# Optimization experiments

Measured on AMD Instinct MI355X. Metric: run time of the kernel, lower is better.

The kernel has to match this reference:

```python
import jax, jax.numpy as jnp
import numpy as np

SCALE_FACTOR = 8.0  # sqrt(head_dim=64)

def setup_inputs() -> dict:
    key = jax.random.key(0)
    kq, kk, kv = jax.random.split(key, 3)
    BH, S, D = 64, 2048, 64  # batch*heads, seq_len, head_dim
    q = jax.random.normal(kq, (BH, S, D), dtype=jnp.float32)
    k = jax.random.normal(kk, (BH, S, D), dtype=jnp.float32)
    v = jax.random.normal(kv, (BH, S, D), dtype=jnp.float32)
    return {"q": q, "k": k, "v": v}

def reference(q, k, v):
    # qk = q @ k^T, scaled, softmax over keys, (dropout p=0 == identity), @ v
    scores = jnp.einsum("bqd,bkd->bqk", q, k) / SCALE_FACTOR  # [BH, S, S]
    attn = jax.nn.softmax(scores, axis=-1)
    out = jnp.einsum("bqk,bkd->bqd", attn, v)  # [BH, S, D]
    return out
```

## Files before the change

### kernel.cpp

```cpp
#include <hip/hip_runtime.h>
#include <hip/hip_bf16.h>


typedef __attribute__((ext_vector_type(8))) short short8;
typedef __attribute__((ext_vector_type(4))) short short4v;
typedef __attribute__((ext_vector_type(4))) float float4v;

#define S_LEN 2048
#define D_DIM 64
#define BH_N  64
#define LOG2E 1.4426950408889634f
#define CLF   (0.125f * LOG2E)

__device__ __forceinline__ unsigned int fpack2_fast(float a, float b) {
    unsigned int ua = __builtin_bit_cast(unsigned int, a) + 0x8000u;
    unsigned int ub = __builtin_bit_cast(unsigned int, b) + 0x8000u;
    return __builtin_amdgcn_perm(ub, ua, 0x07060302);
}
__device__ __forceinline__ unsigned int fpack2_trunc(float a, float b) {
    return __builtin_amdgcn_perm(__builtin_bit_cast(unsigned int, b),
                                 __builtin_bit_cast(unsigned int, a),
                                 0x07060302);
}
__device__ __forceinline__ void load16_lds(const unsigned short* g, unsigned short* l) {
    __builtin_amdgcn_global_load_lds(
        (const __attribute__((address_space(1))) unsigned int*)g,
        (__attribute__((address_space(3))) unsigned int*)l,
        16, 0, 0);
}

__global__ void __launch_bounds__(256) prep(const float* __restrict__ k,
                                            const float* __restrict__ v,
                                            unsigned short* __restrict__ kbf,
                                            unsigned short* __restrict__ vt) {
    __shared__ unsigned short T[64 * 66];
    const int b = blockIdx.x;
    const int t = threadIdx.x;
    if (b & 1) {
        const int kb = b >> 1;
        const size_t i = ((size_t)kb * 256 + t) * 16;
        #pragma unroll
        for (int j = 0; j < 2; ++j) {
            const float4 a0 = *(const float4*)(k + i + j * 8);
            const float4 a1 = *(const float4*)(k + i + j * 8 + 4);
            uint4 o;
            o.x = fpack2_fast(a0.x, a0.y); o.y = fpack2_fast(a0.z, a0.w);
            o.z = fpack2_fast(a1.x, a1.y); o.w = fpack2_fast(a1.z, a1.w);
            *(uint4*)(kbf + i + j * 8) = o;
        }
        return;
    }
    const int idx = b >> 1;
    const int kt = idx & 31, bh = idx >> 5;
    const float* Vg = v + ((size_t)bh * S_LEN + kt * 64) * D_DIM;
    #pragma unroll
    for (int it = 0; it < 4; ++it) {
        const int row = it * 16 + (t >> 4);
        const int col = (t & 15) * 4;
        const float4 f = *(const float4*)(Vg + row * 64 + col);
        unsigned int* p = (unsigned int*)&T[row * 66 + col];
        p[0] = fpack2_fast(f.x, f.y);
        p[1] = fpack2_fast(f.z, f.w);
    }
    __syncthreads();
    const int d  = t >> 2;
    const int kg = t & 3;
    unsigned int w[8];
    #pragma unroll
    for (int j = 0; j < 8; ++j) {
        const unsigned int lo = T[(kg * 16 + 2 * j)     * 66 + d];
        const unsigned int hi = T[(kg * 16 + 2 * j + 1) * 66 + d];
        w[j] = __builtin_amdgcn_perm(hi, lo, 0x05040100);
    }
    unsigned short* out = vt + ((size_t)bh * 64 + d) * S_LEN + kt * 64 + kg * 16;
    uint4 o0; o0.x = w[0]; o0.y = w[1]; o0.z = w[2]; o0.w = w[3];
    uint4 o1; o1.x = w[4]; o1.y = w[5]; o1.z = w[6]; o1.w = w[7];
    *(uint4*)(out)     = o0;
    *(uint4*)(out + 8) = o1;
}

__global__ void __launch_bounds__(256, 4) attn_fwd5(
        const float* __restrict__ q, const unsigned short* __restrict__ kbf,
        const unsigned short* __restrict__ vt, float* __restrict__ out) {
    __shared__ __align__(16) unsigned short Klds[2][64 * 64];
    __shared__ __align__(16) unsigned short Vlds[2][64 * 64];

    const int tid  = threadIdx.x;
    const int lane = tid & 63;
    const int wave = tid >> 6;
    const int l16  = lane & 15;
    const int quad = lane >> 4;
    const int rsw  = l16 & 7;

    const int bh    = blockIdx.y;
    const int qbase = blockIdx.x * 128;

    const unsigned short* Kb = kbf + (size_t)bh * S_LEN * D_DIM;
    const unsigned short* Vb = vt  + (size_t)bh * D_DIM * S_LEN;

    short8 qf[2][2];
    #pragma unroll
    for (int s = 0; s < 2; ++s) {
        const int qg = qbase + s * 64 + wave * 16 + l16;
        const float* Qr = q + ((size_t)bh * S_LEN + qg) * D_DIM;
        #pragma unroll
        for (int h = 0; h < 2; ++h) {
            const float4 a = *(const float4*)(Qr + h * 32 + quad * 8);
            const float4 b = *(const float4*)(Qr + h * 32 + quad * 8 + 4);
            uint4 w;
            w.x = fpack2_fast(a.x * CLF, a.y * CLF);
            w.y = fpack2_fast(a.z * CLF, a.w * CLF);
            w.z = fpack2_fast(b.x * CLF, b.y * CLF);
            w.w = fpack2_fast(b.z * CLF, b.w * CLF);
            qf[s][h] = __builtin_bit_cast(short8, w);
        }
    }

    const int srow0  = wave * 16 + (lane >> 3);
    const int schunk = (lane & 7) ^ (lane >> 3);
    const int dsoff  = wave * 1024 + lane * 8;

    float4v acc[2][4];
    #pragma unroll
    for (int s = 0; s < 2; ++s)
        #pragma unroll
        for (int dt = 0; dt < 4; ++dt) acc[s][dt] = (float4v){0.f, 0.f, 0.f, 0.f};
    float l_acc[2] = {0.f, 0.f};

    auto stage = [&](int kt, int buf) {
        #pragma unroll
        for (int ss = 0; ss < 2; ++ss) {
            const int row = srow0 + ss * 8;
            load16_lds(Kb + ((size_t)(kt * 64 + row)) * 64 + schunk * 8,
                       &Klds[buf][dsoff + ss * 512]);
            load16_lds(Vb + (size_t)row * S_LEN + kt * 64 + schunk * 8,
                       &Vlds[buf][dsoff + ss * 512]);
        }
    };

    auto tile = [&](int buf) {
        float4v st[2][4];
        #pragma unroll
        for (int ks = 0; ks < 4; ++ks) {
            const unsigned short* kr = &Klds[buf][(ks * 16 + l16) * 64];
            const int p0 = ((quad ^ rsw) * 8);
            const short8 kf0 = *(const short8*)(kr + p0);
            const short8 kf1 = *(const short8*)(kr + (p0 ^ 32));
            #pragma unroll
            for (int s = 0; s < 2; ++s) {
                float4v z = (float4v){0.f, 0.f, 0.f, 0.f};
                z = __builtin_amdgcn_mfma_f32_16x16x32_bf16(kf0, qf[s][0], z, 0, 0, 0);
                z = __builtin_amdgcn_mfma_f32_16x16x32_bf16(kf1, qf[s][1], z, 0, 0, 0);
                st[s][ks] = z;
            }
        }
        short4v pf[2][4];
        #pragma unroll
        for (int s = 0; s < 2; ++s) {
            #pragma unroll
            for (int ks = 0; ks < 4; ++ks) {
                const float p0 = __builtin_amdgcn_exp2f(st[s][ks][0]);
                const float p1 = __builtin_amdgcn_exp2f(st[s][ks][1]);
                const float p2 = __builtin_amdgcn_exp2f(st[s][ks][2]);
                const float p3 = __builtin_amdgcn_exp2f(st[s][ks][3]);
                l_acc[s] += (p0 + p1) + (p2 + p3);
                uint2 u; u.x = fpack2_trunc(p0, p1); u.y = fpack2_trunc(p2, p3);
                pf[s][ks] = __builtin_bit_cast(short4v, u);
            }
        }
        #pragma unroll
        for (int dt = 0; dt < 4; ++dt) {
            const unsigned short* vrow = &Vlds[buf][(dt * 16 + l16) * 64 + (quad & 1) * 4];
            #pragma unroll
            for (int ks = 0; ks < 4; ++ks) {
                const int pos16 = (ks * 2 + (quad >> 1)) ^ rsw;
                const short4v vf = *(const short4v*)(vrow + pos16 * 8);
                #pragma unroll
                for (int s = 0; s < 2; ++s)
                    acc[s][dt] = __builtin_amdgcn_mfma_f32_16x16x16bf16_1k(vf, pf[s][ks], acc[s][dt], 0, 0, 0);
            }
        }
    };

    stage(0, 0);
    #pragma unroll 1
    for (int kt = 0; kt < S_LEN / 64; kt += 2) {
        __syncthreads();
        stage(kt + 1, 1);
        tile(0);
        __syncthreads();
        if (kt + 2 < S_LEN / 64) stage(kt + 2, 0);
        tile(1);
    }

    #pragma unroll
    for (int s = 0; s < 2; ++s) {
        float l = l_acc[s];
        l += __shfl_xor(l, 16, 64);
        l += __shfl_xor(l, 32, 64);
        const float inv = 1.0f / l;
        const int qg = qbase + s * 64 + wave * 16 + l16;
        float* Or = out + ((size_t)bh * S_LEN + qg) * D_DIM;
        #pragma unroll
        for (int dt = 0; dt < 4; ++dt) {
            float4 o;
            o.x = acc[s][dt][0] * inv; o.y = acc[s][dt][1] * inv;
            o.z = acc[s][dt][2] * inv; o.w = acc[s][dt][3] * inv;
            *(float4*)(Or + dt * 16 + quad * 4) = o;
        }
    }
}

#define KSTRIDE 72
__global__ void __launch_bounds__(256) attn_fwd(
        const float* __restrict__ q, const float* __restrict__ k,
        const float* __restrict__ v, float* __restrict__ out) {
    __shared__ __align__(16) unsigned short Klds[64 * KSTRIDE];
    __shared__ __align__(16) unsigned short Vlds[64 * KSTRIDE];
    const int tid  = threadIdx.x;
    const int lane = tid & 63;
    const int wave = tid >> 6;
    const int l16  = lane & 15;
    const int quad = lane >> 4;
    const int bh    = blockIdx.y;
    const int qg    = blockIdx.x * 64 + wave * 16 + l16;
    const float* Qr = q + ((size_t)bh * S_LEN + qg) * D_DIM;
    const float* Kb = k + (size_t)bh * S_LEN * D_DIM;
    const float* Vb = v + (size_t)bh * S_LEN * D_DIM;
    short8 qf[2];
    #pragma unroll
    for (int h = 0; h < 2; ++h) {
        const float4 a = *(const float4*)(Qr + h * 32 + quad * 8);
        const float4 b = *(const float4*)(Qr + h * 32 + quad * 8 + 4);
        uint4 w;
        w.x = fpack2_fast(a.x * CLF, a.y * CLF);
        w.y = fpack2_fast(a.z * CLF, a.w * CLF);
        w.z = fpack2_fast(b.x * CLF, b.y * CLF);
        w.w = fpack2_fast(b.z * CLF, b.w * CLF);
        qf[h] = __builtin_bit_cast(short8, w);
    }
    float4v acc[4];
    #pragma unroll
    for (int dt = 0; dt < 4; ++dt) acc[dt] = (float4v){0.f, 0.f, 0.f, 0.f};
    float l_acc = 0.f;
    for (int kt = 0; kt < S_LEN / 64; ++kt) {
        __syncthreads();
        {
            const float* Kg = Kb + (size_t)kt * 64 * D_DIM;
            #pragma unroll
            for (int i = 0; i < 4; ++i) {
                const int idx = tid + i * 256;
                const int row = idx >> 4;
                const int col = (idx & 15) << 2;
                const float4 f = *(const float4*)(Kg + row * 64 + col);
                uint2 w; w.x = fpack2_fast(f.x, f.y); w.y = fpack2_fast(f.z, f.w);
                *(uint2*)(&Klds[row * KSTRIDE + col]) = w;
            }
        }
        {
            const float* Vg = Vb + (size_t)kt * 64 * D_DIM;
            #pragma unroll
            for (int it = 0; it < 2; ++it) {
                const int rp   = (tid & 15) + (it << 4);
                const int cg   = tid >> 4;
                const int row0 = rp * 2;
                const int col  = cg * 4;
                const float4 a = *(const float4*)(Vg + row0 * 64 + col);
                const float4 b = *(const float4*)(Vg + (row0 + 1) * 64 + col);
                *(unsigned int*)(&Vlds[(col + 0) * KSTRIDE + row0]) = fpack2_fast(a.x, b.x);
                *(unsigned int*)(&Vlds[(col + 1) * KSTRIDE + row0]) = fpack2_fast(a.y, b.y);
                *(unsigned int*)(&Vlds[(col + 2) * KSTRIDE + row0]) = fpack2_fast(a.z, b.z);
                *(unsigned int*)(&Vlds[(col + 3) * KSTRIDE + row0]) = fpack2_fast(a.w, b.w);
            }
        }
        __syncthreads();
        float4v st[4];
        #pragma unroll
        for (int ks = 0; ks < 4; ++ks) {
            const unsigned short* kr = &Klds[(ks * 16 + l16) * KSTRIDE + quad * 8];
            const short8 kf0 = *(const short8*)(kr);
            const short8 kf1 = *(const short8*)(kr + 32);
            float4v z = (float4v){0.f, 0.f, 0.f, 0.f};
            z = __builtin_amdgcn_mfma_f32_16x16x32_bf16(kf0, qf[0], z, 0, 0, 0);
            z = __builtin_amdgcn_mfma_f32_16x16x32_bf16(kf1, qf[1], z, 0, 0, 0);
            st[ks] = z;
        }
        short4v pf[4];
        #pragma unroll
        for (int ks = 0; ks < 4; ++ks) {
            const float p0 = __builtin_amdgcn_exp2f(st[ks][0]);
            const float p1 = __builtin_amdgcn_exp2f(st[ks][1]);
            const float p2 = __builtin_amdgcn_exp2f(st[ks][2]);
            const float p3 = __builtin_amdgcn_exp2f(st[ks][3]);
            l_acc += (p0 + p1) + (p2 + p3);
            uint2 u; u.x = fpack2_trunc(p0, p1); u.y = fpack2_trunc(p2, p3);
            pf[ks] = __builtin_bit_cast(short4v, u);
        }
        #pragma unroll
        for (int dt = 0; dt < 4; ++dt) {
            const unsigned short* vr = &Vlds[(dt * 16 + l16) * KSTRIDE + quad * 4];
            #pragma unroll
            for (int ks = 0; ks < 4; ++ks) {
                const short4v vf = *(const short4v*)(vr + ks * 16);
                acc[dt] = __builtin_amdgcn_mfma_f32_16x16x16bf16_1k(vf, pf[ks], acc[dt], 0, 0, 0);
            }
        }
    }
    float l = l_acc;
    l += __shfl_xor(l, 16, 64);
    l += __shfl_xor(l, 32, 64);
    const float inv = 1.0f / l;
    float* Or = out + ((size_t)bh * S_LEN + qg) * D_DIM;
    #pragma unroll
    for (int dt = 0; dt < 4; ++dt) {
        float4 o;
        o.x = acc[dt][0] * inv; o.y = acc[dt][1] * inv;
        o.z = acc[dt][2] * inv; o.w = acc[dt][3] * inv;
        *(float4*)(Or + dt * 16 + quad * 4) = o;
    }
}

extern "C" void kernel_launch(void* const* d_in, const int* in_sizes, int n_in,
                              void* d_out, int out_size, void* d_ws, size_t ws_size,
                              hipStream_t stream) {
    const float* q = (const float*)d_in[0];
    const float* k = (const float*)d_in[1];
    const float* v = (const float*)d_in[2];
    float* out = (float*)d_out;
    const size_t need = (size_t)2 * BH_N * S_LEN * D_DIM * sizeof(unsigned short);
    if (ws_size >= need) {
        unsigned short* kbf = (unsigned short*)d_ws;
        unsigned short* vtp = kbf + (size_t)BH_N * S_LEN * D_DIM;
        prep<<<dim3(4096), 256, 0, stream>>>(k, v, kbf, vtp);
        attn_fwd5<<<dim3(S_LEN / 128, BH_N), 256, 0, stream>>>(q, kbf, vtp, out);
    } else {
        attn_fwd<<<dim3(S_LEN / 64, BH_N), 256, 0, stream>>>(q, k, v, out);
    }
}
```

Before: 217.6 us.

## Drop LDS staging; load K and permuted V fragments directly from global into registers

The attention kernel no longer stages K and V tiles through double-buffered shared memory with barriers. Each wave now loads its own MFMA fragments straight from global memory. The prep kernel writes V-transpose with its keys permuted so that the PV product can use the wider 16x16x32 bf16 MFMA with 8-element fragments in place of 16x16x16. This removes LDS traffic and __syncthreads, but every wave now re-reads K and V from global memory or L2 with no cross-wave sharing and only compiler-driven prefetch.

Result: slower. 447.1 us (+105.5%).

```diff
diff --git a/kernel.cpp b/kernel.cpp
--- a/kernel.cpp
+++ b/kernel.cpp
@@ -21,12 +21,6 @@
     return __builtin_amdgcn_perm(__builtin_bit_cast(unsigned int, b),
                                  __builtin_bit_cast(unsigned int, a),
                                  0x07060302);
-}
-__device__ __forceinline__ void load16_lds(const unsigned short* g, unsigned short* l) {
-    __builtin_amdgcn_global_load_lds(
-        (const __attribute__((address_space(1))) unsigned int*)g,
-        (__attribute__((address_space(3))) unsigned int*)l,
-        16, 0, 0);
 }
 
 __global__ void __launch_bounds__(256) prep(const float* __restrict__ k,
@@ -64,33 +58,32 @@
     }
     __syncthreads();
     const int d  = t >> 2;
-    const int kg = t & 3;
-    unsigned int w[8];
-    #pragma unroll
-    for (int j = 0; j < 8; ++j) {
-        const unsigned int lo = T[(kg * 16 + 2 * j)     * 66 + d];
-        const unsigned int hi = T[(kg * 16 + 2 * j + 1) * 66 + d];
-        w[j] = __builtin_amdgcn_perm(hi, lo, 0x05040100);
-    }
-    unsigned short* out = vt + ((size_t)bh * 64 + d) * S_LEN + kt * 64 + kg * 16;
-    uint4 o0; o0.x = w[0]; o0.y = w[1]; o0.z = w[2]; o0.w = w[3];
-    uint4 o1; o1.x = w[4]; o1.y = w[5]; o1.z = w[6]; o1.w = w[7];
-    *(uint4*)(out)     = o0;
-    *(uint4*)(out + 8) = o1;
-}
-
-__global__ void __launch_bounds__(256, 4) attn_fwd5(
+    const int cg = t & 3;
+    unsigned int w8[8];
+    #pragma unroll
+    for (int cc = 0; cc < 2; ++cc) {
+        const int c   = cg * 2 + cc;
+        const int kb0 = (c >> 2) * 32 + (c & 3) * 4;
+        w8[cc*4+0] = __builtin_amdgcn_perm(T[(kb0+ 1)*66+d], T[(kb0+ 0)*66+d], 0x05040100);
+        w8[cc*4+1] = __builtin_amdgcn_perm(T[(kb0+ 3)*66+d], T[(kb0+ 2)*66+d], 0x05040100);
+        w8[cc*4+2] = __builtin_amdgcn_perm(T[(kb0+17)*66+d], T[(kb0+16)*66+d], 0x05040100);
+        w8[cc*4+3] = __builtin_amdgcn_perm(T[(kb0+19)*66+d], T[(kb0+18)*66+d], 0x05040100);
+    }
+    unsigned short* outp = vt + ((size_t)bh * 64 + d) * S_LEN + kt * 64 + cg * 16;
+    uint4 o0; o0.x = w8[0]; o0.y = w8[1]; o0.z = w8[2]; o0.w = w8[3];
+    uint4 o1; o1.x = w8[4]; o1.y = w8[5]; o1.z = w8[6]; o1.w = w8[7];
+    *(uint4*)(outp)     = o0;
+    *(uint4*)(outp + 8) = o1;
+}
+
+__global__ void __launch_bounds__(256, 4) attn_fwd6(
         const float* __restrict__ q, const unsigned short* __restrict__ kbf,
         const unsigned short* __restrict__ vt, float* __restrict__ out) {
-    __shared__ __align__(16) unsigned short Klds[2][64 * 64];
-    __shared__ __align__(16) unsigned short Vlds[2][64 * 64];
-
     const int tid  = threadIdx.x;
     const int lane = tid & 63;
     const int wave = tid >> 6;
     const int l16  = lane & 15;
     const int quad = lane >> 4;
-    const int rsw  = l16 & 7;
 
     const int bh    = blockIdx.y;
     const int qbase = blockIdx.x * 128;
@@ -116,9 +109,8 @@
         }
     }
 
-    const int srow0  = wave * 16 + (lane >> 3);
-    const int schunk = (lane & 7) ^ (lane >> 3);
-    const int dsoff  = wave * 1024 + lane * 8;
+    const unsigned short* Krow = Kb + (size_t)l16 * 64 + quad * 8;
+    const unsigned short* Vrow = Vb + (size_t)l16 * S_LEN + quad * 8;
 
     float4v acc[2][4];
     #pragma unroll
@@ -127,70 +119,63 @@
         for (int dt = 0; dt < 4; ++dt) acc[s][dt] = (float4v){0.f, 0.f, 0.f, 0.f};
     float l_acc[2] = {0.f, 0.f};
 
-    auto stage = [&](int kt, int buf) {
-        #pragma unroll
-        for (int ss = 0; ss < 2; ++ss) {
-            const int row = srow0 + ss * 8;
-            load16_lds(Kb + ((size_t)(kt * 64 + row)) * 64 + schunk * 8,
-                       &Klds[buf][dsoff + ss * 512]);
-            load16_lds(Vb + (size_t)row * S_LEN + kt * 64 + schunk * 8,
-                       &Vlds[buf][dsoff + ss * 512]);
-        }
-    };
-
-    auto tile = [&](int buf) {
+    #pragma unroll 2
+    for (int kt = 0; kt < S_LEN / 64; ++kt) {
+        const unsigned short* kp = Krow + (size_t)(kt * 64) * 64;
+        short8 kf[4][2];
+        #pragma unroll
+        for (int ks = 0; ks < 4; ++ks) {
+            kf[ks][0] = *(const short8*)(kp + ks * 16 * 64);
+            kf[ks][1] = *(const short8*)(kp + ks * 16 * 64 + 32);
+        }
         float4v st[2][4];
         #pragma unroll
         for (int ks = 0; ks < 4; ++ks) {
-            const unsigned short* kr = &Klds[buf][(ks * 16 + l16) * 64];
-            const int p0 = ((quad ^ rsw) * 8);
-            const short8 kf0 = *(const short8*)(kr + p0);
-            const short8 kf1 = *(const short8*)(kr + (p0 ^ 32));
             #pragma unroll
             for (int s = 0; s < 2; ++s) {
                 float4v z = (float4v){0.f, 0.f, 0.f, 0.f};
-                z = __builtin_amdgcn_mfma_f32_16x16x32_bf16(kf0, qf[s][0], z, 0, 0, 0);
-                z = __builtin_amdgcn_mfma_f32_16x16x32_bf16(kf1, qf[s][1], z, 0, 0, 0);
+                z = __builtin_amdgcn_mfma_f32_16x16x32_bf16(kf[ks][0], qf[s][0], z, 0, 0, 0);
+                z = __builtin_amdgcn_mfma_f32_16x16x32_bf16(kf[ks][1], qf[s][1], z, 0, 0, 0);
                 st[s][ks] = z;
             }
         }
-        short4v pf[2][4];
+        const unsigned short* vp = Vrow + kt * 64;
+        short8 vf[4][2];
+        #pragma unroll
+        for (int dt = 0; dt < 4; ++dt) {
+            #pragma unroll
+            for (int w = 0; w < 2; ++w)
+                vf[dt][w] = *(const short8*)(vp + dt * 16 * S_LEN + w * 32);
+        }
+        short8 pf8[2][2];
         #pragma unroll
         for (int s = 0; s < 2; ++s) {
             #pragma unroll
-            for (int ks = 0; ks < 4; ++ks) {
-                const float p0 = __builtin_amdgcn_exp2f(st[s][ks][0]);
-                const float p1 = __builtin_amdgcn_exp2f(st[s][ks][1]);
-                const float p2 = __builtin_amdgcn_exp2f(st[s][ks][2]);
-                const float p3 = __builtin_amdgcn_exp2f(st[s][ks][3]);
-                l_acc[s] += (p0 + p1) + (p2 + p3);
-                uint2 u; u.x = fpack2_trunc(p0, p1); u.y = fpack2_trunc(p2, p3);
-                pf[s][ks] = __builtin_bit_cast(short4v, u);
+            for (int w = 0; w < 2; ++w) {
+                const float e0 = __builtin_amdgcn_exp2f(st[s][2*w][0]);
+                const float e1 = __builtin_amdgcn_exp2f(st[s][2*w][1]);
+                const float e2 = __builtin_amdgcn_exp2f(st[s][2*w][2]);
+                const float e3 = __builtin_amdgcn_exp2f(st[s][2*w][3]);
+                const float f0 = __builtin_amdgcn_exp2f(st[s][2*w+1][0]);
+                const float f1 = __builtin_amdgcn_exp2f(st[s][2*w+1][1]);
+                const float f2 = __builtin_amdgcn_exp2f(st[s][2*w+1][2]);
+                const float f3 = __builtin_amdgcn_exp2f(st[s][2*w+1][3]);
+                l_acc[s] += ((e0 + e1) + (e2 + e3)) + ((f0 + f1) + (f2 + f3));
+                uint4 u;
+                u.x = fpack2_trunc(e0, e1); u.y = fpack2_trunc(e2, e3);
+                u.z = fpack2_trunc(f0, f1); u.w = fpack2_trunc(f2, f3);
+                pf8[s][w] = __builtin_bit_cast(short8, u);
             }
         }
         #pragma unroll
         for (int dt = 0; dt < 4; ++dt) {
-            const unsigned short* vrow = &Vlds[buf][(dt * 16 + l16) * 64 + (quad & 1) * 4];
-            #pragma unroll
-            for (int ks = 0; ks < 4; ++ks) {
-                const int pos16 = (ks * 2 + (quad >> 1)) ^ rsw;
-                const short4v vf = *(const short4v*)(vrow + pos16 * 8);
+            #pragma unroll
+            for (int w = 0; w < 2; ++w) {
                 #pragma unroll
                 for (int s = 0; s < 2; ++s)
-                    acc[s][dt] = __builtin_amdgcn_mfma_f32_16x16x16bf16_1k(vf, pf[s][ks], acc[s][dt], 0, 0, 0);
-            }
-        }
-    };
-
-    stage(0, 0);
-    #pragma unroll 1
-    for (int kt = 0; kt < S_LEN / 64; kt += 2) {
-        __syncthreads();
-        stage(kt + 1, 1);
-        tile(0);
-        __syncthreads();
-        if (kt + 2 < S_LEN / 64) stage(kt + 2, 0);
-        tile(1);
+                    acc[s][dt] = __builtin_amdgcn_mfma_f32_16x16x32_bf16(vf[dt][w], pf8[s][w], acc[s][dt], 0, 0, 0);
+            }
+        }
     }
 
     #pragma unroll
@@ -332,7 +317,7 @@
         unsigned short* kbf = (unsigned short*)d_ws;
         unsigned short* vtp = kbf + (size_t)BH_N * S_LEN * D_DIM;
         prep<<<dim3(4096), 256, 0, stream>>>(k, v, kbf, vtp);
-        attn_fwd5<<<dim3(S_LEN / 128, BH_N), 256, 0, stream>>>(q, kbf, vtp, out);
+        attn_fwd6<<<dim3(S_LEN / 128, BH_N), 256, 0, stream>>>(q, kbf, vtp, out);
     } else {
         attn_fwd<<<dim3(S_LEN / 64, BH_N), 256, 0, stream>>>(q, k, v, out);
     }
```
